# Performance work log

Hardware: AMD Instinct MI355X
Metric: run time of the kernel (lower is better)

The kernel has to match this reference:

```python
import jax, jax.numpy as jnp
import numpy as np

B, LG = 16, 128            # graphs, nodes per graph
N = B * LG                 # total nodes
LAT, HID, EE, NL = 32, 128, 32, 3
T_STEPS = 100


def setup_inputs() -> dict:
    key = jax.random.key(0)
    ks = list(jax.random.split(key, 64))
    ki = iter(ks)

    def gl(shape):
        fan_in = shape[-2] if len(shape) >= 2 else shape[-1]
        return jax.random.normal(next(ki), shape, dtype=jnp.float32) / np.sqrt(fan_in)

    # ---- graph structure (mirrors FullDPM._get_edges, done under no_grad) ----
    lengths = np.full((B,), LG, dtype=np.int32)
    batch_ids = np.repeat(np.arange(B, dtype=np.int32), LG)
    chain_ids = np.tile((np.arange(LG) >= LG // 2).astype(np.int32), B)  # 2 chains/graph
    rr, cc = np.meshgrid(np.arange(LG), np.arange(LG), indexing='ij')
    offs = (np.arange(B, dtype=np.int64) * LG)[:, None]
    row = (offs + rr.ravel()[None, :]).ravel()
    col = (offs + cc.ravel()[None, :]).ravel()
    is_ctx = chain_ids[row] == chain_ids[col]
    row2 = np.concatenate([row[is_ctx], row[~is_ctx]])
    col2 = np.concatenate([col[is_ctx], col[~is_ctx]])
    edge_types = np.concatenate([np.zeros(is_ctx.sum(), np.int32),
                                 np.ones((~is_ctx).sum(), np.int32)])
    edges = np.stack([row2, col2], axis=0).astype(np.int32)

    inp = {
        'H_0': jax.random.normal(next(ki), (N, LAT), jnp.float32),
        'X_0': jax.random.normal(next(ki), (N, 3), jnp.float32),
        'cond_embedding': jax.random.normal(next(ki), (N, HID), jnp.float32),
        'eps_H': jax.random.normal(next(ki), (N, LAT), jnp.float32),
        'eps_X': jax.random.normal(next(ki), (N, 3), jnp.float32),
        # params: input_mlp MLP(LAT+2*HID -> HID, 3 layers, ReLU)
        'in_W1': gl((LAT + 2 * HID, HID)), 'in_b1': jnp.zeros((HID,)),
        'in_W2': gl((HID, HID)), 'in_b2': jnp.zeros((HID,)),
        'in_W3': gl((HID, HID)), 'in_b3': jnp.zeros((HID,)),
        'edge_emb': gl((2, EE)),
        'h2i_W': gl((HID, LAT)), 'h2i_b': jnp.zeros((LAT,)),
        # EPT encoder (EGNN-style), NL layers stacked
        'pe_W1': gl((NL, 2 * HID + EE + 1, HID)), 'pe_b1': jnp.zeros((NL, HID)),
        'pe_W2': gl((NL, HID, HID)), 'pe_b2': jnp.zeros((NL, HID)),
        'ph_W1': gl((NL, 2 * HID, HID)), 'ph_b1': jnp.zeros((NL, HID)),
        'ph_W2': gl((NL, HID, HID)), 'ph_b2': jnp.zeros((NL, HID)),
        'px_W': gl((NL, HID, 1)), 'px_b': jnp.zeros((NL, 1)),
        # int / bool inputs
        'generate_mask': jax.random.randint(next(ki), (N,), 0, 2) == 1,
        'batch_ids': jnp.asarray(batch_ids),
        'edges': jnp.asarray(edges),
        'edge_types': jnp.asarray(edge_types),
        'lengths': jnp.asarray(lengths),
        't': jax.random.randint(next(ki), (B,), 0, T_STEPS + 1).astype(jnp.int32),
    }
    return inp


def _time_embed(beta, dim):
    half = dim // 2
    freqs = jnp.exp(-jnp.log(jnp.asarray(10000.0, beta.dtype)) *
                    jnp.arange(half, dtype=beta.dtype) / (half - 1))
    args = beta[:, None] * freqs[None, :]
    return jnp.concatenate([jnp.sin(args), jnp.cos(args)], axis=-1)


def reference(H_0, X_0, cond_embedding, eps_H, eps_X,
              in_W1, in_b1, in_W2, in_b2, in_W3, in_b3,
              edge_emb, h2i_W, h2i_b,
              pe_W1, pe_b1, pe_W2, pe_b2,
              ph_W1, ph_b1, ph_W2, ph_b2, px_W, px_b,
              generate_mask, batch_ids, edges, edge_types, lengths, t):
    n = H_0.shape[0]
    maskf = generate_mask[:, None].astype(H_0.dtype)

    # --- DDPM forward noising (trans_x / trans_h .add_noise) ---
    betas = jnp.linspace(1e-4, 0.02, T_STEPS + 1, dtype=H_0.dtype)
    alpha_bar = jnp.cumprod(1.0 - betas)
    ab = alpha_bar[t][batch_ids][:, None]            # (N,1)
    X_noisy = jnp.where(maskf > 0, jnp.sqrt(ab) * X_0 + jnp.sqrt(1.0 - ab) * eps_X, X_0)
    H_noisy = jnp.where(maskf > 0, jnp.sqrt(ab) * H_0 + jnp.sqrt(1.0 - ab) * eps_H, H_0)
    beta_node = betas[t][batch_ids]                  # (N,)

    # --- EpsilonNet ---
    t_emb = _time_embed(beta_node, HID)
    feat = jnp.concatenate([H_noisy, cond_embedding, t_emb], axis=-1)
    h = jax.nn.relu(feat @ in_W1 + in_b1)
    h = jax.nn.relu(h @ in_W2 + in_b2)
    h = h @ in_W3 + in_b3

    e_feat = edge_emb[edge_types]                    # (E, EE)
    row, col = edges[0], edges[1]
    deg = lengths[batch_ids].astype(H_0.dtype)[:, None]  # full per-graph meshgrid degree
    x = X_noisy
    for l in range(NL):
        dvec = x[row] - x[col]                       # (E,3)
        dist2 = jnp.sum(dvec * dvec, axis=-1, keepdims=True)
        m_in = jnp.concatenate([h[row], h[col], e_feat, dist2], axis=-1)
        m = jax.nn.relu(m_in @ pe_W1[l] + pe_b1[l])
        m = jax.nn.relu(m @ pe_W2[l] + pe_b2[l])     # (E, HID)
        agg = jax.ops.segment_sum(m, row, num_segments=n)
        u = jax.nn.relu(jnp.concatenate([h, agg], axis=-1) @ ph_W1[l] + ph_b1[l])
        h = h + u @ ph_W2[l] + ph_b2[l]
        xm = dvec * (m @ px_W[l] + px_b[l])          # (E,3)
        x = x + jax.ops.segment_sum(xm, row, num_segments=n) / deg

    eps_X_pred = (x - X_noisy) * maskf
    eps_H_pred = ((h @ h2i_W + h2i_b) - H_noisy) * maskf

    # --- masked MSE losses ---
    cnt = jnp.sum(generate_mask).astype(H_0.dtype) + 1e-8
    dX = (eps_X_pred - eps_X) * maskf
    dH = (eps_H_pred - eps_H) * maskf
    loss_X = jnp.sum(dX * dX) / cnt
    loss_H = jnp.sum(dH * dH) / cnt
    return jnp.stack([loss_X, loss_H])
```

## Files before the change

### kernel.cpp

```cpp
#include <hip/hip_runtime.h>
#include <math.h>

#define NN 2048
#define NGRAPH 16
#define LG 128
#define LATD 32
#define HIDD 128

typedef __attribute__((ext_vector_type(8))) short short8;
typedef __attribute__((ext_vector_type(4))) float f32x4;

#define OFF_XN   0
#define OFF_HN   (OFF_XN + NN*3)
#define OFF_W2T  (OFF_HN + NN*LATD)
#define OFF_SAB  (OFF_W2T + 24576)
#define OFF_TB   (OFF_SAB + 32)
#define OFF_H    (OFF_TB + NGRAPH*HIDD)
#define OFF_XA   (OFF_H + NN*HIDD)
#define OFF_XB   (OFF_XA + NN*3)
#define OFF_PR   (OFF_XB + NN*3)
#define OFF_PCE0 (OFF_PR + NN*HIDD)
#define OFF_PCE1 (OFF_PCE0 + NN*HIDD)
#define OFF_ACC  (OFF_PCE1 + NN*HIDD)

__device__ __forceinline__ unsigned short f2bf(float f) {
  unsigned u = __float_as_uint(f);
  u += 0x7fffu + ((u >> 16) & 1u);
  return (unsigned short)(u >> 16);
}

__global__ __launch_bounds__(128) void graph_prep_kernel(
    const int* __restrict__ tarr, const float* __restrict__ inW1,
    const float* __restrict__ inb1,
    float* __restrict__ sab, float* __restrict__ tbias, float* __restrict__ acc)
{
  __shared__ float temb[128];
  int g = blockIdx.x;
  int t = threadIdx.x;
  if (g == 0 && t < 4) acc[t] = 0.f;
  int tt = tarr[g];
  float prod = 1.f;
  for (int i=0; i<=tt; ++i) {
    float beta = 1e-4f + 1.99e-4f*(float)i;
    prod *= (1.f - beta);
  }
  float beta_t = 1e-4f + 1.99e-4f*(float)tt;
  if (t == 0) {
    sab[2*g]   = sqrtf(prod);
    sab[2*g+1] = sqrtf(fmaxf(1.f - prod, 0.f));
  }
  if (t < 64) {
    float freq = __expf(-9.210340371976184f * (float)t / 63.f);
    float arg = beta_t * freq;
    temb[t]      = sinf(arg);
    temb[t + 64] = cosf(arg);
  }
  __syncthreads();
  float s = inb1[t];
  for (int k=0;k<128;++k) s += temb[k] * inW1[(160+k)*HIDD + t];
  tbias[g*HIDD + t] = s;
}

__global__ __launch_bounds__(256) void noise_kernel(
    const float* __restrict__ H0, const float* __restrict__ X0,
    const float* __restrict__ epsH, const float* __restrict__ epsX,
    const int* __restrict__ gmask, const float* __restrict__ sab,
    float* __restrict__ Hn, float* __restrict__ Xn, float* __restrict__ xa)
{
  int idx = blockIdx.x*256 + threadIdx.x;
  if (idx < NN*LATD) {
    int n = idx >> 5;
    int g = n >> 7;
    float sa = sab[2*g], sb = sab[2*g+1];
    float v = H0[idx];
    Hn[idx] = gmask[n] ? sa*v + sb*epsH[idx] : v;
  } else {
    int j = idx - NN*LATD;
    if (j < NN*3) {
      int n = j / 3;
      int g = n >> 7;
      float sa = sab[2*g], sb = sab[2*g+1];
      float v = X0[j];
      float xn = gmask[n] ? sa*v + sb*epsX[j] : v;
      Xn[j] = xn;
      xa[j] = xn;
    }
  }
}

__global__ __launch_bounds__(128) void w2t_kernel(
    const float* __restrict__ peW2, unsigned short* __restrict__ w2t)
{
  int l = blockIdx.x;
  int t = threadIdx.x;
  const float* W = peW2 + (size_t)l*HIDD*HIDD;
  unsigned* dst = (unsigned*)(w2t + (size_t)l*HIDD*HIDD);
  for (int k2=0; k2<64; ++k2) {
    float v0 = W[(2*k2)*HIDD + t];
    float v1 = W[(2*k2+1)*HIDD + t];
    dst[t*64 + k2] = (unsigned)f2bf(v0) | ((unsigned)f2bf(v1) << 16);
  }
}

__global__ __launch_bounds__(256) void node_init_kernel(
    const float* __restrict__ Hn, const float* __restrict__ cond,
    const float* __restrict__ tbias, const float* __restrict__ W1,
    const float* __restrict__ W2, const float* __restrict__ b2,
    const float* __restrict__ W3, const float* __restrict__ b3,
    const float* __restrict__ peW1_0, const float* __restrict__ peb1_0,
    const float* __restrict__ eemb,
    float* __restrict__ h, float* __restrict__ Pr, unsigned short* __restrict__ pce)
{
  __shared__ float fL[4][160];
  __shared__ float pbuf[2][4][HIDD];
  __shared__ float h1[4][HIDD];
  __shared__ float h2[4][HIDD];
  __shared__ float hF[4][HIDD];
  int tt = threadIdx.x;
  int nb = blockIdx.x*4;
  int g = nb >> 7;
  int c = tt & 127, half = tt >> 7;
  for (int idx=tt; idx<4*LATD; idx+=256) {
    int nl = idx>>5, k = idx&31;
    fL[nl][k] = Hn[(size_t)nb*LATD + idx];
  }
  for (int idx=tt; idx<4*HIDD; idx+=256) {
    int nl = idx>>7, k = idx&127;
    fL[nl][32+k] = cond[(size_t)nb*HIDD + idx];
  }
  __syncthreads();
  float p[4];
  #pragma unroll
  for (int nl=0;nl<4;++nl) p[nl]=0.f;
  for (int k=half*80; k<half*80+80; ++k) {
    float w = W1[k*HIDD+c];
    #pragma unroll
    for (int nl=0;nl<4;++nl) p[nl] += fL[nl][k]*w;
  }
  #pragma unroll
  for (int nl=0;nl<4;++nl) pbuf[half][nl][c] = p[nl];
  __syncthreads();
  {
    float tb = tbias[g*HIDD + c];
    #pragma unroll
    for (int q=0;q<2;++q) {
      int nl = half*2+q;
      h1[nl][c] = fmaxf(tb + pbuf[0][nl][c] + pbuf[1][nl][c], 0.f);
    }
  }
  __syncthreads();
  #pragma unroll
  for (int nl=0;nl<4;++nl) p[nl]=0.f;
  for (int k=half*64; k<half*64+64; ++k) {
    float w = W2[k*HIDD+c];
    #pragma unroll
    for (int nl=0;nl<4;++nl) p[nl] += h1[nl][k]*w;
  }
  #pragma unroll
  for (int nl=0;nl<4;++nl) pbuf[half][nl][c] = p[nl];
  __syncthreads();
  #pragma unroll
  for (int q=0;q<2;++q) {
    int nl = half*2+q;
    h2[nl][c] = fmaxf(b2[c] + pbuf[0][nl][c] + pbuf[1][nl][c], 0.f);
  }
  __syncthreads();
  #pragma unroll
  for (int nl=0;nl<4;++nl) p[nl]=0.f;
  for (int k=half*64; k<half*64+64; ++k) {
    float w = W3[k*HIDD+c];
    #pragma unroll
    for (int nl=0;nl<4;++nl) p[nl] += h2[nl][k]*w;
  }
  #pragma unroll
  for (int nl=0;nl<4;++nl) pbuf[half][nl][c] = p[nl];
  __syncthreads();
  #pragma unroll
  for (int q=0;q<2;++q) {
    int nl = half*2+q;
    float v = b3[c] + pbuf[0][nl][c] + pbuf[1][nl][c];
    hF[nl][c] = v;
    h[(size_t)(nb+nl)*HIDD+c] = v;
  }
  __syncthreads();
  const float* W = peW1_0 + half*HIDD*HIDD;
  float a[4];
  #pragma unroll
  for (int nl=0;nl<4;++nl) a[nl]=0.f;
  for (int k=0;k<HIDD;++k) {
    float w = W[k*HIDD+c];
    #pragma unroll
    for (int nl=0;nl<4;++nl) a[nl] += hF[nl][k]*w;
  }
  if (half == 0) {
    #pragma unroll
    for (int nl=0;nl<4;++nl) Pr[(size_t)(nb+nl)*HIDD+c] = a[nl];
  } else {
    float e0 = peb1_0[c], e1 = peb1_0[c];
    for (int k=0;k<32;++k) {
      float w = peW1_0[(256+k)*HIDD+c];
      e0 += eemb[k]*w;
      e1 += eemb[32+k]*w;
    }
    #pragma unroll
    for (int nl=0;nl<4;++nl) {
      pce[((size_t)(nb+nl))*HIDD + c]      = f2bf(a[nl] + e0);
      pce[((size_t)(NN + nb+nl))*HIDD + c] = f2bf(a[nl] + e1);
    }
  }
}

__device__ __forceinline__ short8 buildA(uint4 p, f32x4 prA, f32x4 prB,
                                         f32x4 wdA, f32x4 wdB, float d2) {
  float s[8];
  unsigned pu[4] = {p.x, p.y, p.z, p.w};
  #pragma unroll
  for (int q=0;q<4;++q) {
    float lo = __uint_as_float(pu[q] << 16);
    float hi = __uint_as_float(pu[q] & 0xffff0000u);
    float pr0 = (q<2) ? prA[2*q]   : prB[2*q-4];
    float pr1 = (q<2) ? prA[2*q+1] : prB[2*q-3];
    float wd0 = (q<2) ? wdA[2*q]   : wdB[2*q-4];
    float wd1 = (q<2) ? wdA[2*q+1] : wdB[2*q-3];
    s[2*q]   = fmaxf(pr0 + lo + d2*wd0, 0.f);
    s[2*q+1] = fmaxf(pr1 + hi + d2*wd1, 0.f);
  }
  uint4 r;
  asm("v_cvt_pk_bf16_f32 %0, %1, %2" : "=v"(r.x) : "v"(s[0]), "v"(s[1]));
  asm("v_cvt_pk_bf16_f32 %0, %1, %2" : "=v"(r.y) : "v"(s[2]), "v"(s[3]));
  asm("v_cvt_pk_bf16_f32 %0, %1, %2" : "=v"(r.z) : "v"(s[4]), "v"(s[5]));
  asm("v_cvt_pk_bf16_f32 %0, %1, %2" : "=v"(r.w) : "v"(s[6]), "v"(s[7]));
  return *(short8*)&r;
}

template<bool NEXT>
__global__ __launch_bounds__(256, 3) void layer_kernel(
    const float* __restrict__ xR, float* __restrict__ xW,
    float* __restrict__ Pr,
    const unsigned short* __restrict__ pceR, unsigned short* __restrict__ pceW,
    const unsigned short* __restrict__ w2t,
    const float* __restrict__ peW1l, const float* __restrict__ peb2l,
    const float* __restrict__ pxWl, const float* __restrict__ pxbl,
    float* __restrict__ hbuf,
    const float* __restrict__ phW1l, const float* __restrict__ phb1l,
    const float* __restrict__ phW2l, const float* __restrict__ phb2l,
    const float* __restrict__ peW1n, const float* __restrict__ peb1n,
    const float* __restrict__ eemb, const int* __restrict__ lengths)
{
  __shared__ __align__(16) unsigned short W2s[HIDD*HIDD];
  __shared__ __align__(16) float PrL[4][HIDD];
  __shared__ __align__(16) float W1dL[HIDD];
  __shared__ float b2L[HIDD];
  __shared__ float pxWL[HIDD];
  __shared__ float xgL[LG][3];
  __shared__ float SxL[3];
  __shared__ float aggAll[4][HIDD];
  __shared__ float xmAll[4][3];
  __shared__ float hL[4][HIDD];
  __shared__ float uL[4][HIDD];
  __shared__ float hN[4][HIDD];
  __shared__ float partU[2][4][HIDD];
  __shared__ float EFbL[2][HIDD];

  int tt = threadIdx.x;
  int bid = blockIdx.x;
  int g = bid >> 5, ib = bid & 31;
  int i0 = ib*4;
  int nbase = g*LG;

  int w = tt >> 6, l = tt & 63;
  int l15 = l & 15, lg2 = l >> 4;
  int i = i0 + w;

  {
    int col = tt & 127, kh = tt >> 7;
    const uint4* src = (const uint4*)(w2t + (size_t)col*HIDD + kh*64);
    #pragma unroll
    for (int c8=0;c8<8;++c8) {
      uint4 v = src[c8];
      int koff2 = (kh*64 + c8*8)*2;
      int byteoff = col*256 + (koff2 ^ ((col&7)<<4));
      *(uint4*)((char*)W2s + byteoff) = v;
    }
  }
  if (tt < HIDD) {
    W1dL[tt] = peW1l[288*HIDD + tt];
    b2L[tt]  = peb2l[tt];
    pxWL[tt] = pxWl[tt];
  }
  for (int idx=tt; idx<LG*3; idx+=256)
    ((float*)xgL)[idx] = xR[(size_t)nbase*3 + idx];
  for (int idx=l; idx<HIDD; idx+=64)
    PrL[w][idx] = Pr[(size_t)(nbase+i)*HIDD + idx];
  __syncthreads();
  if (tt < 3) {
    float s = 0.f;
    for (int j=0;j<LG;++j) s += xgL[j][tt];
    SxL[tt] = s;
  }
  float pxb0 = pxbl[0];

  float xi0 = xgL[i][0], xi1 = xgL[i][1], xi2 = xgL[i][2];
  int ci = (i >= 64) ? 1 : 0;
  float colsum[8];
  #pragma unroll
  for (int cf=0;cf<8;++cf) colsum[cf] = 0.f;
  float xmx = 0.f, xmy = 0.f, xmz = 0.f;

  for (int jp=0; jp<4; ++jp) {
    int j0 = jp*32 + l15, j1 = j0 + 16;
    float dxa = xi0 - xgL[j0][0], dya = xi1 - xgL[j0][1], dza = xi2 - xgL[j0][2];
    float d2a = dxa*dxa + dya*dya + dza*dza;
    float dxb = xi0 - xgL[j1][0], dyb = xi1 - xgL[j1][1], dzb = xi2 - xgL[j1][2];
    float d2b = dxb*dxb + dyb*dyb + dzb*dzb;
    int et0 = (ci != ((j0 >= 64) ? 1 : 0)) ? 1 : 0;
    int et1 = (ci != ((j1 >= 64) ? 1 : 0)) ? 1 : 0;
    const unsigned short* pceB0 = pceR + ((size_t)(et0*NN + nbase + j0))*HIDD;
    const unsigned short* pceB1 = pceR + ((size_t)(et1*NN + nbase + j1))*HIDD;

    short8 a0[4], a1[4];
    #pragma unroll
    for (int kk=0;kk<4;++kk) {
      int ks = kk*32 + lg2*8;
      f32x4 prA = *(const f32x4*)&PrL[w][ks];
      f32x4 prB = *(const f32x4*)&PrL[w][ks+4];
      f32x4 wdA = *(const f32x4*)&W1dL[ks];
      f32x4 wdB = *(const f32x4*)&W1dL[ks+4];
      uint4 pa = *(const uint4*)(pceB0 + ks);
      uint4 pb = *(const uint4*)(pceB1 + ks);
      a0[kk] = buildA(pa, prA, prB, wdA, wdB, d2a);
      a1[kk] = buildA(pb, prA, prB, wdA, wdB, d2b);
    }

    f32x4 zz = {0.f,0.f,0.f,0.f};
    f32x4 acc[2][8];
    #pragma unroll
    for (int r=0;r<2;++r)
      #pragma unroll
      for (int cf=0;cf<8;++cf) acc[r][cf] = zz;

    #pragma unroll
    for (int kk=0;kk<4;++kk) {
      int kbyte = kk*64 + lg2*16;
      #pragma unroll
      for (int cf=0;cf<8;++cf) {
        int col = cf*16 + l15;
        int boff = col*256 + (kbyte ^ ((col&7)<<4));
        short8 bF = *(const short8*)((const char*)W2s + boff);
        acc[0][cf] = __builtin_amdgcn_mfma_f32_16x16x32_bf16(a0[kk], bF, acc[0][cf], 0,0,0);
        acc[1][cf] = __builtin_amdgcn_mfma_f32_16x16x32_bf16(a1[kk], bF, acc[1][cf], 0,0,0);
      }
    }

    float pxp[2][4];
    #pragma unroll
    for (int r=0;r<2;++r)
      #pragma unroll
      for (int q=0;q<4;++q) pxp[r][q] = 0.f;
    #pragma unroll
    for (int cf=0;cf<8;++cf) {
      int col = cf*16 + l15;
      float b2v = b2L[col], pxv = pxWL[col];
      #pragma unroll
      for (int r=0;r<2;++r)
        #pragma unroll
        for (int q=0;q<4;++q) {
          float m = fmaxf(acc[r][cf][q] + b2v, 0.f);
          colsum[cf] += m;
          pxp[r][q] += m * pxv;
        }
    }
    #pragma unroll
    for (int r=0;r<2;++r)
      #pragma unroll
      for (int q=0;q<4;++q) {
        int row = jp*32 + r*16 + lg2*4 + q;
        float p = pxp[r][q];
        xmx += p*(xi0 - xgL[row][0]);
        xmy += p*(xi1 - xgL[row][1]);
        xmz += p*(xi2 - xgL[row][2]);
      }
  }

  #pragma unroll
  for (int cf=0;cf<8;++cf) {
    float v = colsum[cf];
    v += __shfl_xor(v, 16);
    v += __shfl_xor(v, 32);
    if (l < 16) aggAll[w][cf*16 + l15] = v;
  }
  #pragma unroll
  for (int s=1; s<64; s<<=1) {
    xmx += __shfl_xor(xmx, s);
    xmy += __shfl_xor(xmy, s);
    xmz += __shfl_xor(xmz, s);
  }
  if (l == 0) { xmAll[w][0] = xmx; xmAll[w][1] = xmy; xmAll[w][2] = xmz; }

  int c = tt & 127, half = tt >> 7;
  for (int idx=tt; idx<4*HIDD; idx+=256)
    ((float*)hL)[idx] = hbuf[(size_t)(nbase+i0)*HIDD + idx];
  if (NEXT) {
    int e = half;
    float s = peb1n[c];
    for (int k=0;k<32;++k) s += eemb[e*32+k]*peW1n[(256+k)*HIDD+c];
    EFbL[e][c] = s;
  }
  __syncthreads();

  float p[4];
  {
    const float (*cat)[HIDD] = half ? aggAll : hL;
    #pragma unroll
    for (int nl=0;nl<4;++nl) p[nl]=0.f;
    const float* Wb = phW1l + (size_t)(half*HIDD)*HIDD + c;
    for (int k=0;k<HIDD;++k) {
      float wv = Wb[k*HIDD];
      #pragma unroll
      for (int nl=0;nl<4;++nl) p[nl] += cat[nl][k]*wv;
    }
    #pragma unroll
    for (int nl=0;nl<4;++nl) partU[half][nl][c] = p[nl];
  }
  __syncthreads();
  #pragma unroll
  for (int q=0;q<2;++q) {
    int nl = half*2+q;
    uL[nl][c] = fmaxf(phb1l[c] + partU[0][nl][c] + partU[1][nl][c], 0.f);
  }
  __syncthreads();
  {
    #pragma unroll
    for (int nl=0;nl<4;++nl) p[nl]=0.f;
    const float* Wb = phW2l + (size_t)(half*64)*HIDD + c;
    for (int k=0;k<64;++k) {
      float wv = Wb[k*HIDD];
      #pragma unroll
      for (int nl=0;nl<4;++nl) p[nl] += uL[nl][half*64+k]*wv;
    }
    #pragma unroll
    for (int nl=0;nl<4;++nl) partU[half][nl][c] = p[nl];
  }
  __syncthreads();
  #pragma unroll
  for (int q=0;q<2;++q) {
    int nl = half*2+q;
    float hn = hL[nl][c] + phb2l[c] + partU[0][nl][c] + partU[1][nl][c];
    hN[nl][c] = hn;
    hbuf[(size_t)(nbase+i0+nl)*HIDD+c] = hn;
  }
  __syncthreads();
  if (NEXT) {
    const float* W = peW1n + (size_t)half*HIDD*HIDD;
    float a[4];
    #pragma unroll
    for (int nl=0;nl<4;++nl) a[nl]=0.f;
    for (int k=0;k<HIDD;++k) {
      float wv = W[k*HIDD+c];
      #pragma unroll
      for (int nl=0;nl<4;++nl) a[nl] += hN[nl][k]*wv;
    }
    if (half == 0) {
      #pragma unroll
      for (int nl=0;nl<4;++nl) Pr[(size_t)(nbase+i0+nl)*HIDD+c] = a[nl];
    } else {
      float e0 = EFbL[0][c], e1 = EFbL[1][c];
      #pragma unroll
      for (int nl=0;nl<4;++nl) {
        pceW[((size_t)(nbase+i0+nl))*HIDD + c]      = f2bf(a[nl] + e0);
        pceW[((size_t)(NN + nbase+i0+nl))*HIDD + c] = f2bf(a[nl] + e1);
      }
    }
  }
  if (tt < 12) {
    int nl = tt/3, cc = tt%3;
    int ii = i0 + nl;
    float deg = (float)lengths[g];
    float xmv = xmAll[nl][cc] + pxb0*(128.f*xgL[ii][cc] - SxL[cc]);
    xW[(size_t)(nbase+ii)*3 + cc] = xgL[ii][cc] + xmv/deg;
  }
}

__global__ __launch_bounds__(256) void loss_kernel(
    const float* __restrict__ h, const float* __restrict__ h2iW,
    const float* __restrict__ h2ib, const float* __restrict__ Hn,
    const float* __restrict__ Xn, const float* __restrict__ xf,
    const float* __restrict__ epsH, const float* __restrict__ epsX,
    const int* __restrict__ gmask, float* __restrict__ acc)
{
  __shared__ float hL[8][HIDD];
  __shared__ float rX[256], rH[256], rC[256];
  int tt = threadIdx.x;
  int nb = blockIdx.x*8;
  for (int idx=tt; idx<8*HIDD; idx+=256)
    ((float*)hL)[idx] = h[(size_t)nb*HIDD + idx];
  __syncthreads();
  int nl = tt>>5, c = tt&31;
  int n = nb+nl;
  float mf = gmask[n] ? 1.f : 0.f;
  float pj = h2ib[c];
  for (int k=0;k<HIDD;++k) pj += hL[nl][k]*h2iW[k*LATD+c];
  float dH = mf*((pj - Hn[n*LATD+c]) - epsH[n*LATD+c]);
  float sH = dH*dH;
  float sX = 0.f, sc = 0.f;
  if (c < 3) {
    float dX = mf*((xf[n*3+c]-Xn[n*3+c]) - epsX[n*3+c]);
    sX = dX*dX;
  }
  if (c == 0) sc = mf;
  rX[tt]=sX; rH[tt]=sH; rC[tt]=sc;
  __syncthreads();
  for (int s=128; s>0; s>>=1) {
    if (tt<s) { rX[tt]+=rX[tt+s]; rH[tt]+=rH[tt+s]; rC[tt]+=rC[tt+s]; }
    __syncthreads();
  }
  if (tt==0) {
    atomicAdd(&acc[0], rX[0]);
    atomicAdd(&acc[1], rH[0]);
    atomicAdd(&acc[2], rC[0]);
  }
}

__global__ void finalize_kernel(const float* __restrict__ acc, float* __restrict__ out) {
  if (threadIdx.x==0) {
    float cnt = acc[2] + 1e-8f;
    out[0] = acc[0]/cnt;
    out[1] = acc[1]/cnt;
  }
}

extern "C" void kernel_launch(void* const* d_in, const int* in_sizes, int n_in,
                              void* d_out, int out_size, void* d_ws, size_t ws_size,
                              hipStream_t stream) {
  (void)in_sizes; (void)n_in; (void)out_size; (void)ws_size;
  const float* H0    = (const float*)d_in[0];
  const float* X0    = (const float*)d_in[1];
  const float* cond  = (const float*)d_in[2];
  const float* epsH  = (const float*)d_in[3];
  const float* epsX  = (const float*)d_in[4];
  const float* inW1  = (const float*)d_in[5];
  const float* inb1  = (const float*)d_in[6];
  const float* inW2  = (const float*)d_in[7];
  const float* inb2  = (const float*)d_in[8];
  const float* inW3  = (const float*)d_in[9];
  const float* inb3  = (const float*)d_in[10];
  const float* eemb  = (const float*)d_in[11];
  const float* h2iW  = (const float*)d_in[12];
  const float* h2ib  = (const float*)d_in[13];
  const float* peW1  = (const float*)d_in[14];
  const float* peb1  = (const float*)d_in[15];
  const float* peW2  = (const float*)d_in[16];
  const float* peb2  = (const float*)d_in[17];
  const float* phW1  = (const float*)d_in[18];
  const float* phb1  = (const float*)d_in[19];
  const float* phW2  = (const float*)d_in[20];
  const float* phb2  = (const float*)d_in[21];
  const float* pxW   = (const float*)d_in[22];
  const float* pxB   = (const float*)d_in[23];
  const int* gmask   = (const int*)d_in[24];
  const int* batch   = (const int*)d_in[25];
  (void)batch;
  const int* lengths = (const int*)d_in[28];
  const int* tarr    = (const int*)d_in[29];

  float* ws  = (float*)d_ws;
  float* out = (float*)d_out;
  float* Xn   = ws + OFF_XN;
  float* Hn   = ws + OFF_HN;
  unsigned short* w2tb = (unsigned short*)(ws + OFF_W2T);
  float* sabb = ws + OFF_SAB;
  float* tbb  = ws + OFF_TB;
  float* hbuf = ws + OFF_H;
  float* Xa   = ws + OFF_XA;
  float* Xb   = ws + OFF_XB;
  float* Prb  = ws + OFF_PR;
  unsigned short* pce0 = (unsigned short*)(ws + OFF_PCE0);
  unsigned short* pce1 = (unsigned short*)(ws + OFF_PCE1);
  float* accb = ws + OFF_ACC;

  graph_prep_kernel<<<NGRAPH, 128, 0, stream>>>(tarr, inW1, inb1, sabb, tbb, accb);
  noise_kernel<<<(NN*LATD + NN*3 + 255)/256, 256, 0, stream>>>(
      H0, X0, epsH, epsX, gmask, sabb, Hn, Xn, Xa);
  w2t_kernel<<<3, 128, 0, stream>>>(peW2, w2tb);
  node_init_kernel<<<NN/4, 256, 0, stream>>>(
      Hn, cond, tbb, inW1, inW2, inb2, inW3, inb3,
      peW1, peb1, eemb, hbuf, Prb, pce0);

  layer_kernel<true><<<NGRAPH*32, 256, 0, stream>>>(
      Xa, Xb, Prb, pce0, pce1, w2tb + 0*(size_t)HIDD*HIDD,
      peW1 + 0*(size_t)289*HIDD, peb2 + 0*HIDD, pxW + 0*HIDD, pxB + 0,
      hbuf, phW1 + 0*(size_t)256*HIDD, phb1 + 0*HIDD,
      phW2 + 0*(size_t)HIDD*HIDD, phb2 + 0*HIDD,
      peW1 + 1*(size_t)289*HIDD, peb1 + 1*HIDD, eemb, lengths);
  layer_kernel<true><<<NGRAPH*32, 256, 0, stream>>>(
      Xb, Xa, Prb, pce1, pce0, w2tb + 1*(size_t)HIDD*HIDD,
      peW1 + 1*(size_t)289*HIDD, peb2 + 1*HIDD, pxW + 1*HIDD, pxB + 1,
      hbuf, phW1 + 1*(size_t)256*HIDD, phb1 + 1*HIDD,
      phW2 + 1*(size_t)HIDD*HIDD, phb2 + 1*HIDD,
      peW1 + 2*(size_t)289*HIDD, peb1 + 2*HIDD, eemb, lengths);
  layer_kernel<false><<<NGRAPH*32, 256, 0, stream>>>(
      Xa, Xb, Prb, pce0, nullptr, w2tb + 2*(size_t)HIDD*HIDD,
      peW1 + 2*(size_t)289*HIDD, peb2 + 2*HIDD, pxW + 2*HIDD, pxB + 2,
      hbuf, phW1 + 2*(size_t)256*HIDD, phb1 + 2*HIDD,
      phW2 + 2*(size_t)HIDD*HIDD, phb2 + 2*HIDD,
      nullptr, nullptr, eemb, lengths);

  loss_kernel<<<NN/8, 256, 0, stream>>>(hbuf, h2iW, h2ib, Hn, Xn, Xb,
                                        epsH, epsX, gmask, accb);
  finalize_kernel<<<1, 64, 0, stream>>>(accb, out);
}
```

Measured before the change: 259.6 us.

## Split each node's edge loop across two waves with 512-thread layer blocks

Each layer block now has 512 threads, and two waves share one destination node, each covering half of the neighbour range. Partial aggregates are combined through shared-memory atomics, and coordinate messages through per-wave partials. The node-update MLPs are re-split so each thread handles two nodes instead of four. The aim is to double per-block parallelism and cut per-thread serial work in the edge and update phases, at the cost of more threads competing for registers per CU and extra atomic and sync overhead.

```diff
diff --git a/kernel.cpp b/kernel.cpp
--- a/kernel.cpp
+++ b/kernel.cpp
@@ -234,7 +234,7 @@
 }
 
 template<bool NEXT>
-__global__ __launch_bounds__(256, 3) void layer_kernel(
+__global__ __launch_bounds__(512, 6) void layer_kernel(
     const float* __restrict__ xR, float* __restrict__ xW,
     float* __restrict__ Pr,
     const unsigned short* __restrict__ pceR, unsigned short* __restrict__ pceW,
@@ -255,10 +255,9 @@
   __shared__ float xgL[LG][3];
   __shared__ float SxL[3];
   __shared__ float aggAll[4][HIDD];
-  __shared__ float xmAll[4][3];
+  __shared__ float xmP[8][3];
   __shared__ float hL[4][HIDD];
   __shared__ float uL[4][HIDD];
-  __shared__ float hN[4][HIDD];
   __shared__ float partU[2][4][HIDD];
   __shared__ float EFbL[2][HIDD];
 
@@ -268,17 +267,18 @@
   int i0 = ib*4;
   int nbase = g*LG;
 
-  int w = tt >> 6, l = tt & 63;
+  int wv = tt >> 6, l = tt & 63;
   int l15 = l & 15, lg2 = l >> 4;
-  int i = i0 + w;
+  int iLocal = wv >> 1, jh = wv & 1;
+  int i = i0 + iLocal;
 
   {
     int col = tt & 127, kh = tt >> 7;
-    const uint4* src = (const uint4*)(w2t + (size_t)col*HIDD + kh*64);
-    #pragma unroll
-    for (int c8=0;c8<8;++c8) {
+    const uint4* src = (const uint4*)(w2t + (size_t)col*HIDD) + kh*4;
+    #pragma unroll
+    for (int c8=0;c8<4;++c8) {
       uint4 v = src[c8];
-      int koff2 = (kh*64 + c8*8)*2;
+      int koff2 = ((kh*4 + c8)*8)*2;
       int byteoff = col*256 + (koff2 ^ ((col&7)<<4));
       *(uint4*)((char*)W2s + byteoff) = v;
     }
@@ -288,10 +288,13 @@
     b2L[tt]  = peb2l[tt];
     pxWL[tt] = pxWl[tt];
   }
-  for (int idx=tt; idx<LG*3; idx+=256)
+  for (int idx=tt; idx<LG*3; idx+=512)
     ((float*)xgL)[idx] = xR[(size_t)nbase*3 + idx];
-  for (int idx=l; idx<HIDD; idx+=64)
-    PrL[w][idx] = Pr[(size_t)(nbase+i)*HIDD + idx];
+  {
+    int pr_n = tt >> 7, pr_c = tt & 127;
+    PrL[pr_n][pr_c] = Pr[(size_t)(nbase + i0 + pr_n)*HIDD + pr_c];
+    ((float*)aggAll)[tt] = 0.f;
+  }
   __syncthreads();
   if (tt < 3) {
     float s = 0.f;
@@ -307,7 +310,8 @@
   for (int cf=0;cf<8;++cf) colsum[cf] = 0.f;
   float xmx = 0.f, xmy = 0.f, xmz = 0.f;
 
-  for (int jp=0; jp<4; ++jp) {
+  for (int jj=0; jj<2; ++jj) {
+    int jp = jh*2 + jj;
     int j0 = jp*32 + l15, j1 = j0 + 16;
     float dxa = xi0 - xgL[j0][0], dya = xi1 - xgL[j0][1], dza = xi2 - xgL[j0][2];
     float d2a = dxa*dxa + dya*dya + dza*dza;
@@ -322,8 +326,8 @@
     #pragma unroll
     for (int kk=0;kk<4;++kk) {
       int ks = kk*32 + lg2*8;
-      f32x4 prA = *(const f32x4*)&PrL[w][ks];
-      f32x4 prB = *(const f32x4*)&PrL[w][ks+4];
+      f32x4 prA = *(const f32x4*)&PrL[iLocal][ks];
+      f32x4 prB = *(const f32x4*)&PrL[iLocal][ks+4];
       f32x4 wdA = *(const f32x4*)&W1dL[ks];
       f32x4 wdB = *(const f32x4*)&W1dL[ks+4];
       uint4 pa = *(const uint4*)(pceB0 + ks);
@@ -387,7 +391,7 @@
     float v = colsum[cf];
     v += __shfl_xor(v, 16);
     v += __shfl_xor(v, 32);
-    if (l < 16) aggAll[w][cf*16 + l15] = v;
+    if (l < 16) atomicAdd(&aggAll[iLocal][cf*16 + l15], v);
   }
   #pragma unroll
   for (int s=1; s<64; s<<=1) {
@@ -395,12 +399,17 @@
     xmy += __shfl_xor(xmy, s);
     xmz += __shfl_xor(xmz, s);
   }
-  if (l == 0) { xmAll[w][0] = xmx; xmAll[w][1] = xmy; xmAll[w][2] = xmz; }
-
-  int c = tt & 127, half = tt >> 7;
-  for (int idx=tt; idx<4*HIDD; idx+=256)
-    ((float*)hL)[idx] = hbuf[(size_t)(nbase+i0)*HIDD + idx];
-  if (NEXT) {
+  if (l == 0) { xmP[wv][0] = xmx; xmP[wv][1] = xmy; xmP[wv][2] = xmz; }
+
+  int grp = tt >> 8;
+  int within = tt & 255;
+  int c = within & 127, half = within >> 7;
+  int n0 = grp*2;
+  {
+    int hl_n = tt >> 7, hl_c = tt & 127;
+    hL[hl_n][hl_c] = hbuf[(size_t)(nbase + i0 + hl_n)*HIDD + hl_c];
+  }
+  if (NEXT && grp == 0) {
     int e = half;
     float s = peb1n[c];
     for (int k=0;k<32;++k) s += eemb[e*32+k]*peW1n[(256+k)*HIDD+c];
@@ -408,67 +417,62 @@
   }
   __syncthreads();
 
-  float p[4];
+  float p[2];
   {
     const float (*cat)[HIDD] = half ? aggAll : hL;
-    #pragma unroll
-    for (int nl=0;nl<4;++nl) p[nl]=0.f;
+    p[0] = 0.f; p[1] = 0.f;
     const float* Wb = phW1l + (size_t)(half*HIDD)*HIDD + c;
     for (int k=0;k<HIDD;++k) {
-      float wv = Wb[k*HIDD];
-      #pragma unroll
-      for (int nl=0;nl<4;++nl) p[nl] += cat[nl][k]*wv;
-    }
-    #pragma unroll
-    for (int nl=0;nl<4;++nl) partU[half][nl][c] = p[nl];
-  }
-  __syncthreads();
-  #pragma unroll
-  for (int q=0;q<2;++q) {
-    int nl = half*2+q;
-    uL[nl][c] = fmaxf(phb1l[c] + partU[0][nl][c] + partU[1][nl][c], 0.f);
-  }
-  __syncthreads();
-  {
-    #pragma unroll
-    for (int nl=0;nl<4;++nl) p[nl]=0.f;
+      float wvv = Wb[k*HIDD];
+      p[0] += cat[n0][k]*wvv;
+      p[1] += cat[n0+1][k]*wvv;
+    }
+    partU[half][n0][c] = p[0];
+    partU[half][n0+1][c] = p[1];
+  }
+  __syncthreads();
+  {
+    int nl = tt >> 7, cc = tt & 127;
+    uL[nl][cc] = fmaxf(phb1l[cc] + partU[0][nl][cc] + partU[1][nl][cc], 0.f);
+  }
+  __syncthreads();
+  {
+    p[0] = 0.f; p[1] = 0.f;
     const float* Wb = phW2l + (size_t)(half*64)*HIDD + c;
     for (int k=0;k<64;++k) {
-      float wv = Wb[k*HIDD];
-      #pragma unroll
-      for (int nl=0;nl<4;++nl) p[nl] += uL[nl][half*64+k]*wv;
-    }
-    #pragma unroll
-    for (int nl=0;nl<4;++nl) partU[half][nl][c] = p[nl];
-  }
-  __syncthreads();
-  #pragma unroll
-  for (int q=0;q<2;++q) {
-    int nl = half*2+q;
-    float hn = hL[nl][c] + phb2l[c] + partU[0][nl][c] + partU[1][nl][c];
-    hN[nl][c] = hn;
-    hbuf[(size_t)(nbase+i0+nl)*HIDD+c] = hn;
+      float wvv = Wb[k*HIDD];
+      p[0] += uL[n0][half*64+k]*wvv;
+      p[1] += uL[n0+1][half*64+k]*wvv;
+    }
+    partU[half][n0][c] = p[0];
+    partU[half][n0+1][c] = p[1];
+  }
+  __syncthreads();
+  {
+    int nl = tt >> 7, cc = tt & 127;
+    float hn = hL[nl][cc] + phb2l[cc] + partU[0][nl][cc] + partU[1][nl][cc];
+    hL[nl][cc] = hn;
+    hbuf[(size_t)(nbase+i0+nl)*HIDD+cc] = hn;
   }
   __syncthreads();
   if (NEXT) {
     const float* W = peW1n + (size_t)half*HIDD*HIDD;
-    float a[4];
-    #pragma unroll
-    for (int nl=0;nl<4;++nl) a[nl]=0.f;
+    float a[2];
+    a[0] = 0.f; a[1] = 0.f;
     for (int k=0;k<HIDD;++k) {
-      float wv = W[k*HIDD+c];
-      #pragma unroll
-      for (int nl=0;nl<4;++nl) a[nl] += hN[nl][k]*wv;
+      float wvv = W[k*HIDD+c];
+      a[0] += hL[n0][k]*wvv;
+      a[1] += hL[n0+1][k]*wvv;
     }
     if (half == 0) {
       #pragma unroll
-      for (int nl=0;nl<4;++nl) Pr[(size_t)(nbase+i0+nl)*HIDD+c] = a[nl];
+      for (int q=0;q<2;++q) Pr[(size_t)(nbase+i0+n0+q)*HIDD+c] = a[q];
     } else {
       float e0 = EFbL[0][c], e1 = EFbL[1][c];
       #pragma unroll
-      for (int nl=0;nl<4;++nl) {
-        pceW[((size_t)(nbase+i0+nl))*HIDD + c]      = f2bf(a[nl] + e0);
-        pceW[((size_t)(NN + nbase+i0+nl))*HIDD + c] = f2bf(a[nl] + e1);
+      for (int q=0;q<2;++q) {
+        pceW[((size_t)(nbase+i0+n0+q))*HIDD + c]      = f2bf(a[q] + e0);
+        pceW[((size_t)(NN + nbase+i0+n0+q))*HIDD + c] = f2bf(a[q] + e1);
       }
     }
   }
@@ -476,7 +480,7 @@
     int nl = tt/3, cc = tt%3;
     int ii = i0 + nl;
     float deg = (float)lengths[g];
-    float xmv = xmAll[nl][cc] + pxb0*(128.f*xgL[ii][cc] - SxL[cc]);
+    float xmv = xmP[2*nl][cc] + xmP[2*nl+1][cc] + pxb0*(128.f*xgL[ii][cc] - SxL[cc]);
     xW[(size_t)(nbase+ii)*3 + cc] = xgL[ii][cc] + xmv/deg;
   }
 }
@@ -586,19 +590,19 @@
       Hn, cond, tbb, inW1, inW2, inb2, inW3, inb3,
       peW1, peb1, eemb, hbuf, Prb, pce0);
 
-  layer_kernel<true><<<NGRAPH*32, 256, 0, stream>>>(
+  layer_kernel<true><<<NGRAPH*32, 512, 0, stream>>>(
       Xa, Xb, Prb, pce0, pce1, w2tb + 0*(size_t)HIDD*HIDD,
       peW1 + 0*(size_t)289*HIDD, peb2 + 0*HIDD, pxW + 0*HIDD, pxB + 0,
       hbuf, phW1 + 0*(size_t)256*HIDD, phb1 + 0*HIDD,
       phW2 + 0*(size_t)HIDD*HIDD, phb2 + 0*HIDD,
       peW1 + 1*(size_t)289*HIDD, peb1 + 1*HIDD, eemb, lengths);
-  layer_kernel<true><<<NGRAPH*32, 256, 0, stream>>>(
+  layer_kernel<true><<<NGRAPH*32, 512, 0, stream>>>(
       Xb, Xa, Prb, pce1, pce0, w2tb + 1*(size_t)HIDD*HIDD,
       peW1 + 1*(size_t)289*HIDD, peb2 + 1*HIDD, pxW + 1*HIDD, pxB + 1,
       hbuf, phW1 + 1*(size_t)256*HIDD, phb1 + 1*HIDD,
       phW2 + 1*(size_t)HIDD*HIDD, phb2 + 1*HIDD,
       peW1 + 2*(size_t)289*HIDD, peb1 + 2*HIDD, eemb, lengths);
-  layer_kernel<false><<<NGRAPH*32, 256, 0, stream>>>(
+  layer_kernel<false><<<NGRAPH*32, 512, 0, stream>>>(
       Xa, Xb, Prb, pce0, nullptr, w2tb + 2*(size_t)HIDD*HIDD,
       peW1 + 2*(size_t)289*HIDD, peb2 + 2*HIDD, pxW + 2*HIDD, pxB + 2,
       hbuf, phW1 + 2*(size_t)256*HIDD, phb1 + 2*HIDD,
```

After: 485.4 us. 1.87x slower.

## Stage per-graph pce rows in swizzled LDS and add unroll pragmas

Applied to the files above, without the earlier changes.

Each layer_kernel block now loads the 128 bf16 pce rows for its graph into a 32KB XOR-swizzled shared buffer once. The edge-type variant of each row is chosen from the block's chain. The edge MLP then reads neighbour features from LDS instead of issuing per-edge global loads, and the buffer is reused afterwards as scratch for hL, uL and partU. Unroll pragmas are added to many scalar dot-product loops across the kernels. The larger shared footprint per block may lower how many blocks fit on a CU.

```diff
diff --git a/kernel.cpp b/kernel.cpp
--- a/kernel.cpp
+++ b/kernel.cpp
@@ -57,6 +57,7 @@
   }
   __syncthreads();
   float s = inb1[t];
+  #pragma unroll 8
   for (int k=0;k<128;++k) s += temb[k] * inW1[(160+k)*HIDD + t];
   tbias[g*HIDD + t] = s;
 }
@@ -95,6 +96,7 @@
   int t = threadIdx.x;
   const float* W = peW2 + (size_t)l*HIDD*HIDD;
   unsigned* dst = (unsigned*)(w2t + (size_t)l*HIDD*HIDD);
+  #pragma unroll 4
   for (int k2=0; k2<64; ++k2) {
     float v0 = W[(2*k2)*HIDD + t];
     float v1 = W[(2*k2+1)*HIDD + t];
@@ -132,10 +134,14 @@
   float p[4];
   #pragma unroll
   for (int nl=0;nl<4;++nl) p[nl]=0.f;
-  for (int k=half*80; k<half*80+80; ++k) {
-    float w = W1[k*HIDD+c];
-    #pragma unroll
-    for (int nl=0;nl<4;++nl) p[nl] += fL[nl][k]*w;
+  {
+    int kb = half*80;
+    #pragma unroll 8
+    for (int k=kb; k<kb+80; ++k) {
+      float w = W1[k*HIDD+c];
+      #pragma unroll
+      for (int nl=0;nl<4;++nl) p[nl] += fL[nl][k]*w;
+    }
   }
   #pragma unroll
   for (int nl=0;nl<4;++nl) pbuf[half][nl][c] = p[nl];
@@ -151,10 +157,14 @@
   __syncthreads();
   #pragma unroll
   for (int nl=0;nl<4;++nl) p[nl]=0.f;
-  for (int k=half*64; k<half*64+64; ++k) {
-    float w = W2[k*HIDD+c];
-    #pragma unroll
-    for (int nl=0;nl<4;++nl) p[nl] += h1[nl][k]*w;
+  {
+    int kb = half*64;
+    #pragma unroll 8
+    for (int k=kb; k<kb+64; ++k) {
+      float w = W2[k*HIDD+c];
+      #pragma unroll
+      for (int nl=0;nl<4;++nl) p[nl] += h1[nl][k]*w;
+    }
   }
   #pragma unroll
   for (int nl=0;nl<4;++nl) pbuf[half][nl][c] = p[nl];
@@ -167,10 +177,14 @@
   __syncthreads();
   #pragma unroll
   for (int nl=0;nl<4;++nl) p[nl]=0.f;
-  for (int k=half*64; k<half*64+64; ++k) {
-    float w = W3[k*HIDD+c];
-    #pragma unroll
-    for (int nl=0;nl<4;++nl) p[nl] += h2[nl][k]*w;
+  {
+    int kb = half*64;
+    #pragma unroll 8
+    for (int k=kb; k<kb+64; ++k) {
+      float w = W3[k*HIDD+c];
+      #pragma unroll
+      for (int nl=0;nl<4;++nl) p[nl] += h2[nl][k]*w;
+    }
   }
   #pragma unroll
   for (int nl=0;nl<4;++nl) pbuf[half][nl][c] = p[nl];
@@ -187,6 +201,7 @@
   float a[4];
   #pragma unroll
   for (int nl=0;nl<4;++nl) a[nl]=0.f;
+  #pragma unroll 8
   for (int k=0;k<HIDD;++k) {
     float w = W[k*HIDD+c];
     #pragma unroll
@@ -197,6 +212,7 @@
     for (int nl=0;nl<4;++nl) Pr[(size_t)(nb+nl)*HIDD+c] = a[nl];
   } else {
     float e0 = peb1_0[c], e1 = peb1_0[c];
+    #pragma unroll 8
     for (int k=0;k<32;++k) {
       float w = peW1_0[(256+k)*HIDD+c];
       e0 += eemb[k]*w;
@@ -248,6 +264,7 @@
     const float* __restrict__ eemb, const int* __restrict__ lengths)
 {
   __shared__ __align__(16) unsigned short W2s[HIDD*HIDD];
+  __shared__ __align__(16) char scrS[32768];
   __shared__ __align__(16) float PrL[4][HIDD];
   __shared__ __align__(16) float W1dL[HIDD];
   __shared__ float b2L[HIDD];
@@ -256,10 +273,6 @@
   __shared__ float SxL[3];
   __shared__ float aggAll[4][HIDD];
   __shared__ float xmAll[4][3];
-  __shared__ float hL[4][HIDD];
-  __shared__ float uL[4][HIDD];
-  __shared__ float hN[4][HIDD];
-  __shared__ float partU[2][4][HIDD];
   __shared__ float EFbL[2][HIDD];
 
   int tt = threadIdx.x;
@@ -271,6 +284,7 @@
   int w = tt >> 6, l = tt & 63;
   int l15 = l & 15, lg2 = l >> 4;
   int i = i0 + w;
+  int ci_blk = (i0 >= 64) ? 1 : 0;
 
   {
     int col = tt & 127, kh = tt >> 7;
@@ -283,6 +297,18 @@
       *(uint4*)((char*)W2s + byteoff) = v;
     }
   }
+  {
+    int r = tt & 127, hh = tt >> 7;
+    int et = (ci_blk != ((r >= 64) ? 1 : 0)) ? 1 : 0;
+    const uint4* src = (const uint4*)(pceR + ((size_t)(et*NN + nbase + r))*HIDD) + hh*8;
+    #pragma unroll
+    for (int c8=0;c8<8;++c8) {
+      uint4 v = src[c8];
+      int koff2 = hh*128 + c8*16;
+      int byteoff = r*256 + (koff2 ^ ((r&7)<<4));
+      *(uint4*)(scrS + byteoff) = v;
+    }
+  }
   if (tt < HIDD) {
     W1dL[tt] = peW1l[288*HIDD + tt];
     b2L[tt]  = peb2l[tt];
@@ -301,7 +327,6 @@
   float pxb0 = pxbl[0];
 
   float xi0 = xgL[i][0], xi1 = xgL[i][1], xi2 = xgL[i][2];
-  int ci = (i >= 64) ? 1 : 0;
   float colsum[8];
   #pragma unroll
   for (int cf=0;cf<8;++cf) colsum[cf] = 0.f;
@@ -313,21 +338,18 @@
     float d2a = dxa*dxa + dya*dya + dza*dza;
     float dxb = xi0 - xgL[j1][0], dyb = xi1 - xgL[j1][1], dzb = xi2 - xgL[j1][2];
     float d2b = dxb*dxb + dyb*dyb + dzb*dzb;
-    int et0 = (ci != ((j0 >= 64) ? 1 : 0)) ? 1 : 0;
-    int et1 = (ci != ((j1 >= 64) ? 1 : 0)) ? 1 : 0;
-    const unsigned short* pceB0 = pceR + ((size_t)(et0*NN + nbase + j0))*HIDD;
-    const unsigned short* pceB1 = pceR + ((size_t)(et1*NN + nbase + j1))*HIDD;
 
     short8 a0[4], a1[4];
     #pragma unroll
     for (int kk=0;kk<4;++kk) {
       int ks = kk*32 + lg2*8;
+      int kbyte = kk*64 + lg2*16;
       f32x4 prA = *(const f32x4*)&PrL[w][ks];
       f32x4 prB = *(const f32x4*)&PrL[w][ks+4];
       f32x4 wdA = *(const f32x4*)&W1dL[ks];
       f32x4 wdB = *(const f32x4*)&W1dL[ks+4];
-      uint4 pa = *(const uint4*)(pceB0 + ks);
-      uint4 pb = *(const uint4*)(pceB1 + ks);
+      uint4 pa = *(const uint4*)(scrS + j0*256 + (kbyte ^ ((j0&7)<<4)));
+      uint4 pb = *(const uint4*)(scrS + j1*256 + (kbyte ^ ((j1&7)<<4)));
       a0[kk] = buildA(pa, prA, prB, wdA, wdB, d2a);
       a1[kk] = buildA(pb, prA, prB, wdA, wdB, d2b);
     }
@@ -397,12 +419,18 @@
   }
   if (l == 0) { xmAll[w][0] = xmx; xmAll[w][1] = xmy; xmAll[w][2] = xmz; }
 
+  __syncthreads();
+
+  float* hLp   = (float*)scrS;
+  float* uLp   = hLp + 4*HIDD;
+  float* partU = uLp + 4*HIDD;
   int c = tt & 127, half = tt >> 7;
   for (int idx=tt; idx<4*HIDD; idx+=256)
-    ((float*)hL)[idx] = hbuf[(size_t)(nbase+i0)*HIDD + idx];
+    hLp[idx] = hbuf[(size_t)(nbase+i0)*HIDD + idx];
   if (NEXT) {
     int e = half;
     float s = peb1n[c];
+    #pragma unroll 8
     for (int k=0;k<32;++k) s += eemb[e*32+k]*peW1n[(256+k)*HIDD+c];
     EFbL[e][c] = s;
   }
@@ -410,43 +438,45 @@
 
   float p[4];
   {
-    const float (*cat)[HIDD] = half ? aggAll : hL;
+    const float* cat = half ? &aggAll[0][0] : hLp;
     #pragma unroll
     for (int nl=0;nl<4;++nl) p[nl]=0.f;
     const float* Wb = phW1l + (size_t)(half*HIDD)*HIDD + c;
+    #pragma unroll 8
     for (int k=0;k<HIDD;++k) {
-      float wv = Wb[k*HIDD];
-      #pragma unroll
-      for (int nl=0;nl<4;++nl) p[nl] += cat[nl][k]*wv;
-    }
-    #pragma unroll
-    for (int nl=0;nl<4;++nl) partU[half][nl][c] = p[nl];
+      float wv = Wb[(size_t)k*HIDD];
+      #pragma unroll
+      for (int nl=0;nl<4;++nl) p[nl] += cat[nl*HIDD+k]*wv;
+    }
+    #pragma unroll
+    for (int nl=0;nl<4;++nl) partU[(half*4+nl)*HIDD + c] = p[nl];
   }
   __syncthreads();
   #pragma unroll
   for (int q=0;q<2;++q) {
     int nl = half*2+q;
-    uL[nl][c] = fmaxf(phb1l[c] + partU[0][nl][c] + partU[1][nl][c], 0.f);
+    uLp[nl*HIDD+c] = fmaxf(phb1l[c] + partU[nl*HIDD+c] + partU[(4+nl)*HIDD+c], 0.f);
   }
   __syncthreads();
   {
     #pragma unroll
     for (int nl=0;nl<4;++nl) p[nl]=0.f;
     const float* Wb = phW2l + (size_t)(half*64)*HIDD + c;
+    #pragma unroll 8
     for (int k=0;k<64;++k) {
-      float wv = Wb[k*HIDD];
-      #pragma unroll
-      for (int nl=0;nl<4;++nl) p[nl] += uL[nl][half*64+k]*wv;
-    }
-    #pragma unroll
-    for (int nl=0;nl<4;++nl) partU[half][nl][c] = p[nl];
+      float wv = Wb[(size_t)k*HIDD];
+      #pragma unroll
+      for (int nl=0;nl<4;++nl) p[nl] += uLp[nl*HIDD + half*64+k]*wv;
+    }
+    #pragma unroll
+    for (int nl=0;nl<4;++nl) partU[(half*4+nl)*HIDD + c] = p[nl];
   }
   __syncthreads();
   #pragma unroll
   for (int q=0;q<2;++q) {
     int nl = half*2+q;
-    float hn = hL[nl][c] + phb2l[c] + partU[0][nl][c] + partU[1][nl][c];
-    hN[nl][c] = hn;
+    float hn = hLp[nl*HIDD+c] + phb2l[c] + partU[nl*HIDD+c] + partU[(4+nl)*HIDD+c];
+    hLp[nl*HIDD+c] = hn;
     hbuf[(size_t)(nbase+i0+nl)*HIDD+c] = hn;
   }
   __syncthreads();
@@ -455,10 +485,11 @@
     float a[4];
     #pragma unroll
     for (int nl=0;nl<4;++nl) a[nl]=0.f;
+    #pragma unroll 8
     for (int k=0;k<HIDD;++k) {
       float wv = W[k*HIDD+c];
       #pragma unroll
-      for (int nl=0;nl<4;++nl) a[nl] += hN[nl][k]*wv;
+      for (int nl=0;nl<4;++nl) a[nl] += hLp[nl*HIDD+k]*wv;
     }
     if (half == 0) {
       #pragma unroll
@@ -499,6 +530,7 @@
   int n = nb+nl;
   float mf = gmask[n] ? 1.f : 0.f;
   float pj = h2ib[c];
+  #pragma unroll 8
   for (int k=0;k<HIDD;++k) pj += hL[nl][k]*h2iW[k*LATD+c];
   float dH = mf*((pj - Hn[n*LATD+c]) - epsH[n*LATD+c]);
   float sH = dH*dH;
```

After: 272.9 us. +5.1%, slower.
